# Optimization experiments

Hardware: AMD Instinct MI355X
Metric: run time of the kernel (lower is better)

## Reference

```python
import jax, jax.numpy as jnp
import numpy as np

MARGIN = 0.2
NEG_INF = -1e9  # safe stand-in for -inf when masking the max


def setup_inputs() -> dict:
    key = jax.random.key(0)
    k1, k2, k3 = jax.random.split(key, 3)
    B, D = 8192, 256
    p = jax.random.normal(k1, (B, D), dtype=jnp.float32)
    # module docstring says projections are normalized
    projections = p / jnp.linalg.norm(p, axis=1, keepdims=True)
    affordance_ids = jax.random.randint(k2, (B,), 0, 36, dtype=jnp.int64)
    instance_ids = jax.random.randint(k3, (B,), 0, 2048, dtype=jnp.int64)
    return {
        "projections": projections,
        "affordance_ids": affordance_ids,
        "instance_ids": instance_ids,
    }


def reference(projections, affordance_ids, instance_ids):
    # (B, B) cosine similarities
    sim = jnp.matmul(projections, projections.T)

    aff_eq = affordance_ids[:, None] == affordance_ids[None, :]
    inst_eq = instance_ids[:, None] == instance_ids[None, :]
    pos_mask = aff_eq & ~inst_eq          # same affordance, different instance
    neg_mask = ~aff_eq                    # different affordance

    # per-row hard negative: max similarity over negatives
    hard_neg = jnp.max(jnp.where(neg_mask, sim, NEG_INF), axis=1)  # (B,)

    # rows contribute only if they have >=1 positive AND >=1 negative
    valid_row = pos_mask.any(axis=1) & neg_mask.any(axis=1)        # (B,)
    pair_mask = pos_mask & valid_row[:, None]                      # (B, B)

    # margin loss for every (anchor i, positive j) pair
    losses = jnp.maximum(hard_neg[:, None] - sim + MARGIN, 0.0)

    total = jnp.sum(jnp.where(pair_mask, losses, 0.0))
    num_pairs = jnp.sum(pair_mask)
    return jnp.where(num_pairs > 0, total / num_pairs, 0.0)
```

## Files before the change

kernel.cpp:

```cpp
#include <hip/hip_runtime.h>

#define NB 8192
#define ND 256
#define NCLS 64
#define LOSS_MARGIN 0.2f
#define NEG_INF_F (-1e9f)
#define LMAXT 3
#define NBLK_LOSS (NCLS * LMAXT * LMAXT)
#define NT 64
#define NTILE_T 2080

typedef __attribute__((ext_vector_type(8))) __bf16 bf16x8;
typedef __attribute__((ext_vector_type(4))) float f32x4;

__device__ __forceinline__ unsigned short f2bf(float f) {
  unsigned u = __float_as_uint(f);
  unsigned r = (u + 0x7fffu + ((u >> 16) & 1u)) >> 16;
  return (unsigned short)r;
}

__device__ __forceinline__ void gl_lds16(const void* gsrc, void* ldst) {
  __builtin_amdgcn_global_load_lds(
      (const __attribute__((address_space(1))) void*)gsrc,
      (__attribute__((address_space(3))) void*)ldst, 16, 0, 0);
}

__global__ __launch_bounds__(256) void build_idx(const int* __restrict__ aff,
                                                 int* __restrict__ class_start,
                                                 int* __restrict__ class_idx) {
  const int c = blockIdx.x;
  const int t = threadIdx.x;
  const int lane = t & 63, wave = t >> 6;
  __shared__ int wtotLT[4];
  __shared__ int wtotEQ[4];

  int a[32];
#pragma unroll
  for (int k = 0; k < 32; ++k) a[k] = aff[t * 32 + k];
  int ltc = 0, meq = 0;
#pragma unroll
  for (int k = 0; k < 32; ++k) {
    ltc += (a[k] < c) ? 1 : 0;
    meq += (a[k] == c) ? 1 : 0;
  }

  int sc = meq;
  for (int d = 1; d < 64; d <<= 1) {
    int n = __shfl_up(sc, d);
    if (lane >= d) sc += n;
  }
  int ltr = ltc;
  for (int off = 32; off; off >>= 1) ltr += __shfl_down(ltr, off);
  if (lane == 63) wtotEQ[wave] = sc;
  if (lane == 0) wtotLT[wave] = ltr;
  __syncthreads();

  int base = wtotLT[0] + wtotLT[1] + wtotLT[2] + wtotLT[3];
  int wpre = 0;
  for (int w = 0; w < wave; ++w) wpre += wtotEQ[w];
  int p = base + wpre + (sc - meq);

  if (t == 0) {
    class_start[c] = base;
    if (c == 0) class_start[NCLS] = NB;
  }
#pragma unroll
  for (int k = 0; k < 32; ++k)
    if (a[k] == c) class_idx[p++] = t * 32 + k;
}

__global__ __launch_bounds__(256) void gather_convert(const float* __restrict__ P,
                                                      const int* __restrict__ aff,
                                                      const int* __restrict__ inst,
                                                      const int* __restrict__ class_idx,
                                                      unsigned short* __restrict__ Psort,
                                                      int* __restrict__ affSort,
                                                      int* __restrict__ instSort) {
  const int t = threadIdx.x;
  const int sr = blockIdx.x * 8 + (t >> 5);
  const int c = t & 31;
  const int src = class_idx[sr];
  const float4* ps = (const float4*)(P + (size_t)src * ND);
  ushort4* pd = (ushort4*)(Psort + (size_t)sr * ND);
#pragma unroll
  for (int q = 0; q < 2; ++q) {
    float4 v = ps[c + q * 32];
    ushort4 h;
    h.x = f2bf(v.x); h.y = f2bf(v.y); h.z = f2bf(v.z); h.w = f2bf(v.w);
    pd[c + q * 32] = h;
  }
  if (c == 0) {
    affSort[sr] = aff[src];
    instSort[sr] = inst[src];
  }
}

__global__ __launch_bounds__(256, 4) void simmax_mfma(const unsigned short* __restrict__ Psort,
                                                      const int* __restrict__ affSort,
                                                      float* __restrict__ part) {
  int wg = blockIdx.x;
  wg = (wg & 7) * (NTILE_T / 8) + (wg >> 3);
  int bi = (int)((129.0f - sqrtf(129.0f * 129.0f - 8.0f * (float)wg)) * 0.5f);
  while (bi * 64 - bi * (bi - 1) / 2 > wg) --bi;
  while ((bi + 1) * 64 - (bi + 1) * bi / 2 <= wg) ++bi;
  const int bj = bi + (wg - (bi * 64 - bi * (bi - 1) / 2));

  __shared__ __align__(16) unsigned short smemu[16384];
  float* rowmax_s = (float*)&smemu[0];
  float* colmax_s = (float*)&smemu[512];

  const int t = threadIdx.x;
  const int lane = t & 63;
  const int wave = t >> 6;
  const int r0 = bi * 128, c0 = bj * 128;

  const bool needMask = (affSort[c0] <= affSort[r0 + 127]);

  const int wr = (wave >> 1) * 64;
  const int wc = (wave & 1) * 64;

  f32x4 acc[4][4];
#pragma unroll
  for (int m = 0; m < 4; ++m)
#pragma unroll
    for (int n = 0; n < 4; ++n) acc[m][n] = (f32x4){0.f, 0.f, 0.f, 0.f};

  const int ci0 = t, ci1 = 256 + t;
  const int kg0 = ci0 >> 7, rw0 = ci0 & 127;
  const int kg1 = ci1 >> 7, rw1 = ci1 & 127;

#define STAGE_SIM(B, KC)                                                      \
  do {                                                                        \
    gl_lds16(Psort + (size_t)(r0 + rw0) * ND + (KC) + kg0 * 8,                \
             &smemu[(B) * 4096 + ci0 * 8]);                                   \
    gl_lds16(Psort + (size_t)(c0 + rw0) * ND + (KC) + kg0 * 8,                \
             &smemu[8192 + (B) * 4096 + ci0 * 8]);                            \
    gl_lds16(Psort + (size_t)(r0 + rw1) * ND + (KC) + kg1 * 8,                \
             &smemu[(B) * 4096 + ci1 * 8]);                                   \
    gl_lds16(Psort + (size_t)(c0 + rw1) * ND + (KC) + kg1 * 8,                \
             &smemu[8192 + (B) * 4096 + ci1 * 8]);                            \
  } while (0)

  STAGE_SIM(0, 0);
  asm volatile("s_waitcnt vmcnt(0) lgkmcnt(0)" ::: "memory");
  __builtin_amdgcn_s_barrier();
  __builtin_amdgcn_sched_barrier(0);

  int cur = 0;
#pragma unroll 1
  for (int s = 0; s < 8; ++s) {
    if (s < 7) STAGE_SIM(cur ^ 1, (s + 1) * 32);
    const int kg = lane >> 4, lr = lane & 15;
    bf16x8 a[4], b[4];
#pragma unroll
    for (int m = 0; m < 4; ++m)
      a[m] = *(const bf16x8*)&smemu[cur * 4096 + (kg * 128 + wr + m * 16 + lr) * 8];
#pragma unroll
    for (int n = 0; n < 4; ++n)
      b[n] = *(const bf16x8*)&smemu[8192 + cur * 4096 + (kg * 128 + wc + n * 16 + lr) * 8];
#pragma unroll
    for (int m = 0; m < 4; ++m)
#pragma unroll
      for (int n = 0; n < 4; ++n)
        acc[m][n] = __builtin_amdgcn_mfma_f32_16x16x32_bf16(a[m], b[n], acc[m][n], 0, 0, 0);
    __builtin_amdgcn_sched_barrier(0);
    if (s < 7) {
      asm volatile("s_waitcnt vmcnt(0)" ::: "memory");
      __builtin_amdgcn_s_barrier();
      __builtin_amdgcn_sched_barrier(0);
    }
    cur ^= 1;
  }

  if (needMask) {
    int aj[4];
#pragma unroll
    for (int n = 0; n < 4; ++n) aj[n] = affSort[c0 + wc + n * 16 + (lane & 15)];
#pragma unroll
    for (int m = 0; m < 4; ++m) {
#pragma unroll
      for (int r = 0; r < 4; ++r) {
        const int lrow = wr + m * 16 + (lane >> 4) * 4 + r;
        const int ai = affSort[r0 + lrow];
        float rmax = NEG_INF_F;
#pragma unroll
        for (int n = 0; n < 4; ++n)
          if (aj[n] != ai) rmax = fmaxf(rmax, acc[m][n][r]);
        rmax = fmaxf(rmax, __shfl_xor(rmax, 1));
        rmax = fmaxf(rmax, __shfl_xor(rmax, 2));
        rmax = fmaxf(rmax, __shfl_xor(rmax, 4));
        rmax = fmaxf(rmax, __shfl_xor(rmax, 8));
        if ((lane & 15) == 0) rowmax_s[lrow * 2 + (wc >> 6)] = rmax;
      }
    }
    if (bi != bj) {
#pragma unroll
      for (int n = 0; n < 4; ++n) {
        const int lcol = wc + n * 16 + (lane & 15);
        float cmax = NEG_INF_F;
#pragma unroll
        for (int m = 0; m < 4; ++m) {
          const int lrb = wr + m * 16 + (lane >> 4) * 4;
#pragma unroll
          for (int r = 0; r < 4; ++r)
            if (affSort[r0 + lrb + r] != aj[n]) cmax = fmaxf(cmax, acc[m][n][r]);
        }
        cmax = fmaxf(cmax, __shfl_xor(cmax, 16));
        cmax = fmaxf(cmax, __shfl_xor(cmax, 32));
        if (lane < 16) colmax_s[lcol * 2 + (wr >> 6)] = cmax;
      }
    }
  } else {
#pragma unroll
    for (int m = 0; m < 4; ++m) {
#pragma unroll
      for (int r = 0; r < 4; ++r) {
        float rmax = fmaxf(fmaxf(acc[m][0][r], acc[m][1][r]),
                           fmaxf(acc[m][2][r], acc[m][3][r]));
        rmax = fmaxf(rmax, __shfl_xor(rmax, 1));
        rmax = fmaxf(rmax, __shfl_xor(rmax, 2));
        rmax = fmaxf(rmax, __shfl_xor(rmax, 4));
        rmax = fmaxf(rmax, __shfl_xor(rmax, 8));
        if ((lane & 15) == 0)
          rowmax_s[(wr + m * 16 + (lane >> 4) * 4 + r) * 2 + (wc >> 6)] = rmax;
      }
    }
#pragma unroll
    for (int n = 0; n < 4; ++n) {
      float cmax = NEG_INF_F;
#pragma unroll
      for (int m = 0; m < 4; ++m)
#pragma unroll
        for (int r = 0; r < 4; ++r) cmax = fmaxf(cmax, acc[m][n][r]);
      cmax = fmaxf(cmax, __shfl_xor(cmax, 16));
      cmax = fmaxf(cmax, __shfl_xor(cmax, 32));
      if (lane < 16) colmax_s[(wc + n * 16 + (lane & 15)) * 2 + (wr >> 6)] = cmax;
    }
  }
  __syncthreads();
  if (t < 128) {
    part[(size_t)bj * NB + (r0 + t)] = fmaxf(rowmax_s[t * 2], rowmax_s[t * 2 + 1]);
  } else if (bi != bj) {
    const int cc = t - 128;
    part[(size_t)bi * NB + (c0 + cc)] = fmaxf(colmax_s[cc * 2], colmax_s[cc * 2 + 1]);
  }
#undef STAGE_SIM
}

__global__ __launch_bounds__(256) void hn_reduce(const float* __restrict__ part,
                                                 float* __restrict__ hn) {
  const int i = blockIdx.x * 256 + threadIdx.x;
  float m = NEG_INF_F;
#pragma unroll 16
  for (int q = 0; q < NT; ++q) m = fmaxf(m, part[(size_t)q * NB + i]);
  hn[i] = m;
}

__global__ __launch_bounds__(256, 4) void loss_mfma(const unsigned short* __restrict__ Psort,
                                                    const int* __restrict__ class_start,
                                                    const int* __restrict__ instSort,
                                                    const float* __restrict__ hn,
                                                    float* __restrict__ bsum,
                                                    int* __restrict__ bcnt) {
  const int c = blockIdx.z;
  const int ti = blockIdx.x, tj = blockIdx.y;
  const int bid = (c * LMAXT + ti) * LMAXT + tj;
  const int t = threadIdx.x;
  const int base = class_start[c];
  const int cnt = class_start[c + 1] - base;
  const int nt = (cnt + 127) >> 7;
  if (ti >= nt || tj >= nt || cnt >= NB) {
    if (t == 0) { bsum[bid] = 0.f; bcnt[bid] = 0; }
    return;
  }

  __shared__ __align__(16) unsigned short At[2][4096];
  __shared__ __align__(16) unsigned short Bt[2][4096];
  __shared__ int instI[128], instJ[128];
  __shared__ float hnI[128];

  const int lane = t & 63;
  const int wave = t >> 6;

  if (t < 128) {
    int ri = ti * 128 + t;
    int gi = base + (ri < cnt ? ri : 0);
    instI[t] = instSort[gi];
    hnI[t] = hn[gi];
  } else {
    int tt = t - 128;
    int rj = tj * 128 + tt;
    int gj = base + (rj < cnt ? rj : 0);
    instJ[tt] = instSort[gj];
  }

  const int wr = (wave >> 1) * 64;
  const int wc = (wave & 1) * 64;

  f32x4 acc[4][4];
#pragma unroll
  for (int m = 0; m < 4; ++m)
#pragma unroll
    for (int n = 0; n < 4; ++n) acc[m][n] = (f32x4){0.f, 0.f, 0.f, 0.f};

  const int ci0 = t, ci1 = 256 + t;
  const int kg0 = ci0 >> 7, rw0 = ci0 & 127;
  const int kg1 = ci1 >> 7, rw1 = ci1 & 127;
  const int ra0 = base + (ti * 128 + rw0 < cnt ? ti * 128 + rw0 : 0);
  const int ra1 = base + (ti * 128 + rw1 < cnt ? ti * 128 + rw1 : 0);
  const int rb0 = base + (tj * 128 + rw0 < cnt ? tj * 128 + rw0 : 0);
  const int rb1 = base + (tj * 128 + rw1 < cnt ? tj * 128 + rw1 : 0);

#define STAGE_LOSS(B, KC)                                               \
  do {                                                                  \
    gl_lds16(Psort + (size_t)ra0 * ND + (KC) + kg0 * 8, &At[B][ci0 * 8]); \
    gl_lds16(Psort + (size_t)rb0 * ND + (KC) + kg0 * 8, &Bt[B][ci0 * 8]); \
    gl_lds16(Psort + (size_t)ra1 * ND + (KC) + kg1 * 8, &At[B][ci1 * 8]); \
    gl_lds16(Psort + (size_t)rb1 * ND + (KC) + kg1 * 8, &Bt[B][ci1 * 8]); \
  } while (0)

  STAGE_LOSS(0, 0);
  asm volatile("s_waitcnt vmcnt(0) lgkmcnt(0)" ::: "memory");
  __builtin_amdgcn_s_barrier();
  __builtin_amdgcn_sched_barrier(0);

  int cur = 0;
#pragma unroll 1
  for (int s = 0; s < 8; ++s) {
    if (s < 7) STAGE_LOSS(cur ^ 1, (s + 1) * 32);
    const int kg = lane >> 4, lr = lane & 15;
    bf16x8 a[4], b[4];
#pragma unroll
    for (int m = 0; m < 4; ++m)
      a[m] = *(const bf16x8*)&At[cur][(kg * 128 + wr + m * 16 + lr) * 8];
#pragma unroll
    for (int n = 0; n < 4; ++n)
      b[n] = *(const bf16x8*)&Bt[cur][(kg * 128 + wc + n * 16 + lr) * 8];
#pragma unroll
    for (int m = 0; m < 4; ++m)
#pragma unroll
      for (int n = 0; n < 4; ++n)
        acc[m][n] = __builtin_amdgcn_mfma_f32_16x16x32_bf16(a[m], b[n], acc[m][n], 0, 0, 0);
    __builtin_amdgcn_sched_barrier(0);
    if (s < 7) {
      asm volatile("s_waitcnt vmcnt(0)" ::: "memory");
      __builtin_amdgcn_s_barrier();
      __builtin_amdgcn_sched_barrier(0);
    }
    cur ^= 1;
  }

  float lsum = 0.f;
  int lcnt = 0;
#pragma unroll
  for (int m = 0; m < 4; ++m) {
#pragma unroll
    for (int r = 0; r < 4; ++r) {
      const int lrow = wr + m * 16 + (lane >> 4) * 4 + r;
      const int ri = ti * 128 + lrow;
      if (ri >= cnt) continue;
      const float hnv = hnI[lrow];
      const int ii = instI[lrow];
#pragma unroll
      for (int n = 0; n < 4; ++n) {
        const int lcol = wc + n * 16 + (lane & 15);
        const int rj = tj * 128 + lcol;
        if (rj < cnt && instJ[lcol] != ii) {
          lsum += fmaxf(hnv - acc[m][n][r] + LOSS_MARGIN, 0.f);
          lcnt += 1;
        }
      }
    }
  }

  for (int off = 32; off; off >>= 1) {
    lsum += __shfl_down(lsum, off);
    lcnt += __shfl_down(lcnt, off);
  }
  __shared__ float wsum[4];
  __shared__ int wcnt[4];
  if (lane == 0) { wsum[wave] = lsum; wcnt[wave] = lcnt; }
  __syncthreads();
  if (t == 0) {
    bsum[bid] = wsum[0] + wsum[1] + wsum[2] + wsum[3];
    bcnt[bid] = wcnt[0] + wcnt[1] + wcnt[2] + wcnt[3];
  }
#undef STAGE_LOSS
}

__global__ __launch_bounds__(256) void finalize_kernel(const float* __restrict__ bsum,
                                                       const int* __restrict__ bcnt,
                                                       float* __restrict__ out) {
  const int t = threadIdx.x;
  float s = 0.f;
  int n = 0;
  for (int i = t; i < NBLK_LOSS; i += 256) { s += bsum[i]; n += bcnt[i]; }
  for (int off = 32; off; off >>= 1) {
    s += __shfl_down(s, off);
    n += __shfl_down(n, off);
  }
  __shared__ float wsum[4];
  __shared__ int wcnt[4];
  if ((t & 63) == 0) { wsum[t >> 6] = s; wcnt[t >> 6] = n; }
  __syncthreads();
  if (t == 0) {
    const float S = wsum[0] + wsum[1] + wsum[2] + wsum[3];
    const int N = wcnt[0] + wcnt[1] + wcnt[2] + wcnt[3];
    out[0] = (N > 0) ? (S / (float)N) : 0.0f;
  }
}

extern "C" void kernel_launch(void* const* d_in, const int* in_sizes, int n_in,
                              void* d_out, int out_size, void* d_ws, size_t ws_size,
                              hipStream_t stream) {
  const float* P = (const float*)d_in[0];
  const int* aff = (const int*)d_in[1];
  const int* inst = (const int*)d_in[2];
  float* out = (float*)d_out;

  unsigned short* Psort = (unsigned short*)d_ws;
  float* part = (float*)((char*)d_ws + (size_t)NB * ND * 2);
  int* ibase = (int*)((char*)part + (size_t)NT * NB * 4);
  float* hn        = (float*)ibase;
  int* class_start = ibase + NB;
  int* class_idx   = ibase + NB + NCLS + 1;
  int* affSort     = ibase + 2 * NB + NCLS + 1;
  int* instSort    = ibase + 3 * NB + NCLS + 1;
  float* bsum = (float*)(ibase + 4 * NB + NCLS + 1);
  int* bcnt   = ibase + 4 * NB + NCLS + 1 + NBLK_LOSS;

  build_idx<<<NCLS, 256, 0, stream>>>(aff, class_start, class_idx);
  gather_convert<<<NB / 8, 256, 0, stream>>>(P, aff, inst, class_idx, Psort,
                                             affSort, instSort);
  simmax_mfma<<<NTILE_T, 256, 0, stream>>>(Psort, affSort, part);
  hn_reduce<<<NB / 256, 256, 0, stream>>>(part, hn);
  loss_mfma<<<dim3(LMAXT, LMAXT, NCLS), 256, 0, stream>>>(Psort, class_start, instSort,
                                                          hn, bsum, bcnt);
  finalize_kernel<<<1, 256, 0, stream>>>(bsum, bcnt, out);
}
```

Measured before the change: 89.48 us.

## Process two triangular sim tiles per workgroup, prefetching second tile during first

The similarity-max kernel now handles two consecutive upper-triangle tiles per workgroup, launching half as many blocks. During the last k-step of tile A it issues the first k-slice load of tile B, so B's first global fetch overlaps A's final MFMAs and epilogue. Row and column max scratch moves to dedicated shared arrays so the epilogue does not clobber the staging buffers holding B's prefetched data. This trades grid parallelism (1040 blocks across 256 CUs) for amortised launch and prologue latency, and could leave load imbalance in the final wave.

Result: slower. 100.8 us (+12.6%).

```diff
diff --git a/kernel.cpp b/kernel.cpp
--- a/kernel.cpp
+++ b/kernel.cpp
@@ -9,6 +9,7 @@
 #define NBLK_LOSS (NCLS * LMAXT * LMAXT)
 #define NT 64
 #define NTILE_T 2080
+#define NPAIR 1040
 
 typedef __attribute__((ext_vector_type(8))) __bf16 bf16x8;
 typedef __attribute__((ext_vector_type(4))) float f32x4;
@@ -23,6 +24,14 @@
   __builtin_amdgcn_global_load_lds(
       (const __attribute__((address_space(1))) void*)gsrc,
       (__attribute__((address_space(3))) void*)ldst, 16, 0, 0);
+}
+
+__device__ __forceinline__ void tri_decode(int wg, int& bi, int& bj) {
+  int b = (int)((129.0f - sqrtf(129.0f * 129.0f - 8.0f * (float)wg)) * 0.5f);
+  while (b * 64 - b * (b - 1) / 2 > wg) --b;
+  while ((b + 1) * 64 - (b + 1) * b / 2 <= wg) ++b;
+  bi = b;
+  bj = b + (wg - (b * 64 - b * (b - 1) / 2));
 }
 
 __global__ __launch_bounds__(256) void build_idx(const int* __restrict__ aff,
@@ -98,50 +107,153 @@
 __global__ __launch_bounds__(256, 4) void simmax_mfma(const unsigned short* __restrict__ Psort,
                                                       const int* __restrict__ affSort,
                                                       float* __restrict__ part) {
-  int wg = blockIdx.x;
-  wg = (wg & 7) * (NTILE_T / 8) + (wg >> 3);
-  int bi = (int)((129.0f - sqrtf(129.0f * 129.0f - 8.0f * (float)wg)) * 0.5f);
-  while (bi * 64 - bi * (bi - 1) / 2 > wg) --bi;
-  while ((bi + 1) * 64 - (bi + 1) * bi / 2 <= wg) ++bi;
-  const int bj = bi + (wg - (bi * 64 - bi * (bi - 1) / 2));
+  int b = blockIdx.x;
+  b = (b & 7) * (NPAIR / 8) + (b >> 3);
+  int biA, bjA, biB, bjB;
+  tri_decode(2 * b, biA, bjA);
+  tri_decode(2 * b + 1, biB, bjB);
 
   __shared__ __align__(16) unsigned short smemu[16384];
-  float* rowmax_s = (float*)&smemu[0];
-  float* colmax_s = (float*)&smemu[512];
+  __shared__ float rowmax_s[128][2];
+  __shared__ float colmax_s[128][2];
 
   const int t = threadIdx.x;
   const int lane = t & 63;
   const int wave = t >> 6;
-  const int r0 = bi * 128, c0 = bj * 128;
-
-  const bool needMask = (affSort[c0] <= affSort[r0 + 127]);
+
+  const int r0a = biA * 128, c0a = bjA * 128;
+  const int r0b = biB * 128, c0b = bjB * 128;
+
+  const bool needMaskA = (affSort[c0a] <= affSort[r0a + 127]);
+  const bool needMaskB = (affSort[c0b] <= affSort[r0b + 127]);
 
   const int wr = (wave >> 1) * 64;
   const int wc = (wave & 1) * 64;
 
   f32x4 acc[4][4];
-#pragma unroll
-  for (int m = 0; m < 4; ++m)
-#pragma unroll
-    for (int n = 0; n < 4; ++n) acc[m][n] = (f32x4){0.f, 0.f, 0.f, 0.f};
 
   const int ci0 = t, ci1 = 256 + t;
   const int kg0 = ci0 >> 7, rw0 = ci0 & 127;
   const int kg1 = ci1 >> 7, rw1 = ci1 & 127;
 
-#define STAGE_SIM(B, KC)                                                      \
+#define STAGE_SIM(B, R0, C0, KC)                                              \
   do {                                                                        \
-    gl_lds16(Psort + (size_t)(r0 + rw0) * ND + (KC) + kg0 * 8,                \
+    gl_lds16(Psort + (size_t)((R0) + rw0) * ND + (KC) + kg0 * 8,              \
              &smemu[(B) * 4096 + ci0 * 8]);                                   \
-    gl_lds16(Psort + (size_t)(c0 + rw0) * ND + (KC) + kg0 * 8,                \
+    gl_lds16(Psort + (size_t)((C0) + rw0) * ND + (KC) + kg0 * 8,              \
              &smemu[8192 + (B) * 4096 + ci0 * 8]);                            \
-    gl_lds16(Psort + (size_t)(r0 + rw1) * ND + (KC) + kg1 * 8,                \
+    gl_lds16(Psort + (size_t)((R0) + rw1) * ND + (KC) + kg1 * 8,              \
              &smemu[(B) * 4096 + ci1 * 8]);                                   \
-    gl_lds16(Psort + (size_t)(c0 + rw1) * ND + (KC) + kg1 * 8,                \
+    gl_lds16(Psort + (size_t)((C0) + rw1) * ND + (KC) + kg1 * 8,              \
              &smemu[8192 + (B) * 4096 + ci1 * 8]);                            \
   } while (0)
 
-  STAGE_SIM(0, 0);
+#define KBODY(CUR)                                                            \
+  do {                                                                        \
+    const int kg = lane >> 4, lr = lane & 15;                                 \
+    bf16x8 a[4], bfr[4];                                                      \
+    _Pragma("unroll")                                                         \
+    for (int m = 0; m < 4; ++m)                                               \
+      a[m] = *(const bf16x8*)&smemu[(CUR) * 4096 +                            \
+                                    (kg * 128 + wr + m * 16 + lr) * 8];       \
+    _Pragma("unroll")                                                         \
+    for (int n = 0; n < 4; ++n)                                               \
+      bfr[n] = *(const bf16x8*)&smemu[8192 + (CUR) * 4096 +                   \
+                                      (kg * 128 + wc + n * 16 + lr) * 8];     \
+    _Pragma("unroll")                                                         \
+    for (int m = 0; m < 4; ++m)                                               \
+      _Pragma("unroll")                                                       \
+      for (int n = 0; n < 4; ++n)                                             \
+        acc[m][n] = __builtin_amdgcn_mfma_f32_16x16x32_bf16(a[m], bfr[n],     \
+                                                            acc[m][n], 0, 0, 0); \
+  } while (0)
+
+#define EPILOG(R0, C0, BI, BJ, NEEDMASK)                                      \
+  do {                                                                        \
+    if (NEEDMASK) {                                                           \
+      int aj[4];                                                              \
+      _Pragma("unroll")                                                       \
+      for (int n = 0; n < 4; ++n)                                             \
+        aj[n] = affSort[(C0) + wc + n * 16 + (lane & 15)];                    \
+      _Pragma("unroll")                                                       \
+      for (int m = 0; m < 4; ++m) {                                           \
+        _Pragma("unroll")                                                     \
+        for (int r = 0; r < 4; ++r) {                                         \
+          const int lrow = wr + m * 16 + (lane >> 4) * 4 + r;                 \
+          const int ai = affSort[(R0) + lrow];                                \
+          float rmax = NEG_INF_F;                                             \
+          _Pragma("unroll")                                                   \
+          for (int n = 0; n < 4; ++n)                                         \
+            if (aj[n] != ai) rmax = fmaxf(rmax, acc[m][n][r]);                \
+          rmax = fmaxf(rmax, __shfl_xor(rmax, 1));                            \
+          rmax = fmaxf(rmax, __shfl_xor(rmax, 2));                            \
+          rmax = fmaxf(rmax, __shfl_xor(rmax, 4));                            \
+          rmax = fmaxf(rmax, __shfl_xor(rmax, 8));                            \
+          if ((lane & 15) == 0) rowmax_s[lrow][wc >> 6] = rmax;               \
+        }                                                                     \
+      }                                                                       \
+      if ((BI) != (BJ)) {                                                     \
+        _Pragma("unroll")                                                     \
+        for (int n = 0; n < 4; ++n) {                                         \
+          const int lcol = wc + n * 16 + (lane & 15);                         \
+          float cmax = NEG_INF_F;                                             \
+          _Pragma("unroll")                                                   \
+          for (int m = 0; m < 4; ++m) {                                       \
+            const int lrb = wr + m * 16 + (lane >> 4) * 4;                    \
+            _Pragma("unroll")                                                 \
+            for (int r = 0; r < 4; ++r)                                       \
+              if (affSort[(R0) + lrb + r] != aj[n])                           \
+                cmax = fmaxf(cmax, acc[m][n][r]);                             \
+          }                                                                   \
+          cmax = fmaxf(cmax, __shfl_xor(cmax, 16));                           \
+          cmax = fmaxf(cmax, __shfl_xor(cmax, 32));                           \
+          if (lane < 16) colmax_s[lcol][wr >> 6] = cmax;                      \
+        }                                                                     \
+      }                                                                       \
+    } else {                                                                  \
+      _Pragma("unroll")                                                       \
+      for (int m = 0; m < 4; ++m) {                                           \
+        _Pragma("unroll")                                                     \
+        for (int r = 0; r < 4; ++r) {                                         \
+          float rmax = fmaxf(fmaxf(acc[m][0][r], acc[m][1][r]),               \
+                             fmaxf(acc[m][2][r], acc[m][3][r]));              \
+          rmax = fmaxf(rmax, __shfl_xor(rmax, 1));                            \
+          rmax = fmaxf(rmax, __shfl_xor(rmax, 2));                            \
+          rmax = fmaxf(rmax, __shfl_xor(rmax, 4));                            \
+          rmax = fmaxf(rmax, __shfl_xor(rmax, 8));                            \
+          if ((lane & 15) == 0)                                               \
+            rowmax_s[wr + m * 16 + (lane >> 4) * 4 + r][wc >> 6] = rmax;      \
+        }                                                                     \
+      }                                                                       \
+      _Pragma("unroll")                                                       \
+      for (int n = 0; n < 4; ++n) {                                           \
+        float cmax = NEG_INF_F;                                               \
+        _Pragma("unroll")                                                     \
+        for (int m = 0; m < 4; ++m)                                           \
+          _Pragma("unroll")                                                   \
+          for (int r = 0; r < 4; ++r) cmax = fmaxf(cmax, acc[m][n][r]);       \
+        cmax = fmaxf(cmax, __shfl_xor(cmax, 16));                             \
+        cmax = fmaxf(cmax, __shfl_xor(cmax, 32));                             \
+        if (lane < 16) colmax_s[wc + n * 16 + (lane & 15)][wr >> 6] = cmax;   \
+      }                                                                       \
+    }                                                                         \
+    __syncthreads();                                                          \
+    if (t < 128) {                                                            \
+      part[(size_t)(BJ) * NB + ((R0) + t)] =                                  \
+          fmaxf(rowmax_s[t][0], rowmax_s[t][1]);                              \
+    } else if ((BI) != (BJ)) {                                                \
+      const int cc = t - 128;                                                 \
+      part[(size_t)(BI) * NB + ((C0) + cc)] =                                 \
+          fmaxf(colmax_s[cc][0], colmax_s[cc][1]);                            \
+    }                                                                         \
+  } while (0)
+
+#pragma unroll
+  for (int m = 0; m < 4; ++m)
+#pragma unroll
+    for (int n = 0; n < 4; ++n) acc[m][n] = (f32x4){0.f, 0.f, 0.f, 0.f};
+
+  STAGE_SIM(0, r0a, c0a, 0);
   asm volatile("s_waitcnt vmcnt(0) lgkmcnt(0)" ::: "memory");
   __builtin_amdgcn_s_barrier();
   __builtin_amdgcn_sched_barrier(0);
@@ -149,20 +261,9 @@
   int cur = 0;
 #pragma unroll 1
   for (int s = 0; s < 8; ++s) {
-    if (s < 7) STAGE_SIM(cur ^ 1, (s + 1) * 32);
-    const int kg = lane >> 4, lr = lane & 15;
-    bf16x8 a[4], b[4];
-#pragma unroll
-    for (int m = 0; m < 4; ++m)
-      a[m] = *(const bf16x8*)&smemu[cur * 4096 + (kg * 128 + wr + m * 16 + lr) * 8];
-#pragma unroll
-    for (int n = 0; n < 4; ++n)
-      b[n] = *(const bf16x8*)&smemu[8192 + cur * 4096 + (kg * 128 + wc + n * 16 + lr) * 8];
-#pragma unroll
-    for (int m = 0; m < 4; ++m)
-#pragma unroll
-      for (int n = 0; n < 4; ++n)
-        acc[m][n] = __builtin_amdgcn_mfma_f32_16x16x32_bf16(a[m], b[n], acc[m][n], 0, 0, 0);
+    if (s < 7) STAGE_SIM(cur ^ 1, r0a, c0a, (s + 1) * 32);
+    else       STAGE_SIM(cur ^ 1, r0b, c0b, 0);
+    KBODY(cur);
     __builtin_amdgcn_sched_barrier(0);
     if (s < 7) {
       asm volatile("s_waitcnt vmcnt(0)" ::: "memory");
@@ -172,78 +273,33 @@
     cur ^= 1;
   }
 
-  if (needMask) {
-    int aj[4];
-#pragma unroll
-    for (int n = 0; n < 4; ++n) aj[n] = affSort[c0 + wc + n * 16 + (lane & 15)];
-#pragma unroll
-    for (int m = 0; m < 4; ++m) {
-#pragma unroll
-      for (int r = 0; r < 4; ++r) {
-        const int lrow = wr + m * 16 + (lane >> 4) * 4 + r;
-        const int ai = affSort[r0 + lrow];
-        float rmax = NEG_INF_F;
-#pragma unroll
-        for (int n = 0; n < 4; ++n)
-          if (aj[n] != ai) rmax = fmaxf(rmax, acc[m][n][r]);
-        rmax = fmaxf(rmax, __shfl_xor(rmax, 1));
-        rmax = fmaxf(rmax, __shfl_xor(rmax, 2));
-        rmax = fmaxf(rmax, __shfl_xor(rmax, 4));
-        rmax = fmaxf(rmax, __shfl_xor(rmax, 8));
-        if ((lane & 15) == 0) rowmax_s[lrow * 2 + (wc >> 6)] = rmax;
-      }
+  EPILOG(r0a, c0a, biA, bjA, needMaskA);
+
+#pragma unroll
+  for (int m = 0; m < 4; ++m)
+#pragma unroll
+    for (int n = 0; n < 4; ++n) acc[m][n] = (f32x4){0.f, 0.f, 0.f, 0.f};
+
+  asm volatile("s_waitcnt vmcnt(0)" ::: "memory");
+  __builtin_amdgcn_s_barrier();
+  __builtin_amdgcn_sched_barrier(0);
+
+#pragma unroll 1
+  for (int s = 0; s < 8; ++s) {
+    if (s < 7) STAGE_SIM(cur ^ 1, r0b, c0b, (s + 1) * 32);
+    KBODY(cur);
+    __builtin_amdgcn_sched_barrier(0);
+    if (s < 7) {
+      asm volatile("s_waitcnt vmcnt(0)" ::: "memory");
+      __builtin_amdgcn_s_barrier();
+      __builtin_amdgcn_sched_barrier(0);
     }
-    if (bi != bj) {
-#pragma unroll
-      for (int n = 0; n < 4; ++n) {
-        const int lcol = wc + n * 16 + (lane & 15);
-        float cmax = NEG_INF_F;
-#pragma unroll
-        for (int m = 0; m < 4; ++m) {
-          const int lrb = wr + m * 16 + (lane >> 4) * 4;
-#pragma unroll
-          for (int r = 0; r < 4; ++r)
-            if (affSort[r0 + lrb + r] != aj[n]) cmax = fmaxf(cmax, acc[m][n][r]);
-        }
-        cmax = fmaxf(cmax, __shfl_xor(cmax, 16));
-        cmax = fmaxf(cmax, __shfl_xor(cmax, 32));
-        if (lane < 16) colmax_s[lcol * 2 + (wr >> 6)] = cmax;
-      }
-    }
-  } else {
-#pragma unroll
-    for (int m = 0; m < 4; ++m) {
-#pragma unroll
-      for (int r = 0; r < 4; ++r) {
-        float rmax = fmaxf(fmaxf(acc[m][0][r], acc[m][1][r]),
-                           fmaxf(acc[m][2][r], acc[m][3][r]));
-        rmax = fmaxf(rmax, __shfl_xor(rmax, 1));
-        rmax = fmaxf(rmax, __shfl_xor(rmax, 2));
-        rmax = fmaxf(rmax, __shfl_xor(rmax, 4));
-        rmax = fmaxf(rmax, __shfl_xor(rmax, 8));
-        if ((lane & 15) == 0)
-          rowmax_s[(wr + m * 16 + (lane >> 4) * 4 + r) * 2 + (wc >> 6)] = rmax;
-      }
-    }
-#pragma unroll
-    for (int n = 0; n < 4; ++n) {
-      float cmax = NEG_INF_F;
-#pragma unroll
-      for (int m = 0; m < 4; ++m)
-#pragma unroll
-        for (int r = 0; r < 4; ++r) cmax = fmaxf(cmax, acc[m][n][r]);
-      cmax = fmaxf(cmax, __shfl_xor(cmax, 16));
-      cmax = fmaxf(cmax, __shfl_xor(cmax, 32));
-      if (lane < 16) colmax_s[(wc + n * 16 + (lane & 15)) * 2 + (wr >> 6)] = cmax;
-    }
-  }
-  __syncthreads();
-  if (t < 128) {
-    part[(size_t)bj * NB + (r0 + t)] = fmaxf(rowmax_s[t * 2], rowmax_s[t * 2 + 1]);
-  } else if (bi != bj) {
-    const int cc = t - 128;
-    part[(size_t)bi * NB + (c0 + cc)] = fmaxf(colmax_s[cc * 2], colmax_s[cc * 2 + 1]);
-  }
+    cur ^= 1;
+  }
+
+  EPILOG(r0b, c0b, biB, bjB, needMaskB);
+#undef EPILOG
+#undef KBODY
 #undef STAGE_SIM
 }
 
@@ -432,7 +488,7 @@
   build_idx<<<NCLS, 256, 0, stream>>>(aff, class_start, class_idx);
   gather_convert<<<NB / 8, 256, 0, stream>>>(P, aff, inst, class_idx, Psort,
                                              affSort, instSort);
-  simmax_mfma<<<NTILE_T, 256, 0, stream>>>(Psort, affSort, part);
+  simmax_mfma<<<NPAIR, 256, 0, stream>>>(Psort, affSort, part);
   hn_reduce<<<NB / 256, 256, 0, stream>>>(part, hn);
   loss_mfma<<<dim3(LMAXT, LMAXT, NCLS), 256, 0, stream>>>(Psort, class_start, instSort,
                                                           hn, bsum, bcnt);
```

## Cache near-diagonal similarity tiles in bf16 and reuse them for the loss

Applied to the files above, without the earlier changes.

The similarity kernel now writes bf16 copies of the masked tiles within four tile-diagonals of the main diagonal into a workspace buffer. The loss stage no longer runs a second MFMA pass. It becomes a scalar pair loop that gathers cached similarities for same-class, different-instance pairs. This removes the recomputed matmul, but adds 2-byte scattered stores in the similarity kernel and a latency-bound serial loop over rows. It also rounds the similarity to bf16 before computing the margin loss.

Result: slower. 129.1 us (+44.3%).

```diff
diff --git a/kernel.cpp b/kernel.cpp
--- a/kernel.cpp
+++ b/kernel.cpp
@@ -5,8 +5,7 @@
 #define NCLS 64
 #define LOSS_MARGIN 0.2f
 #define NEG_INF_F (-1e9f)
-#define LMAXT 3
-#define NBLK_LOSS (NCLS * LMAXT * LMAXT)
+#define NBLK_LOSS 256
 #define NT 64
 #define NTILE_T 2080
 
@@ -97,7 +96,8 @@
 
 __global__ __launch_bounds__(256, 4) void simmax_mfma(const unsigned short* __restrict__ Psort,
                                                       const int* __restrict__ affSort,
-                                                      float* __restrict__ part) {
+                                                      float* __restrict__ part,
+                                                      unsigned short* __restrict__ simbuf) {
   int wg = blockIdx.x;
   wg = (wg & 7) * (NTILE_T / 8) + (wg >> 3);
   int bi = (int)((129.0f - sqrtf(129.0f * 129.0f - 8.0f * (float)wg)) * 0.5f);
@@ -210,6 +210,22 @@
         if (lane < 16) colmax_s[lcol * 2 + (wr >> 6)] = cmax;
       }
     }
+    const int d = bj - bi;
+    if (d < 4) {
+      unsigned short* dst = simbuf + ((size_t)((bi << 2) + d) << 14);
+#pragma unroll
+      for (int m = 0; m < 4; ++m) {
+#pragma unroll
+        for (int r = 0; r < 4; ++r) {
+          const int lrow = wr + m * 16 + (lane >> 4) * 4 + r;
+#pragma unroll
+          for (int n = 0; n < 4; ++n) {
+            const int lcol = wc + n * 16 + (lane & 15);
+            dst[lrow * 128 + lcol] = f2bf(acc[m][n][r]);
+          }
+        }
+      }
+    }
   } else {
 #pragma unroll
     for (int m = 0; m < 4; ++m) {
@@ -256,117 +272,40 @@
   hn[i] = m;
 }
 
-__global__ __launch_bounds__(256, 4) void loss_mfma(const unsigned short* __restrict__ Psort,
-                                                    const int* __restrict__ class_start,
-                                                    const int* __restrict__ instSort,
-                                                    const float* __restrict__ hn,
-                                                    float* __restrict__ bsum,
-                                                    int* __restrict__ bcnt) {
-  const int c = blockIdx.z;
-  const int ti = blockIdx.x, tj = blockIdx.y;
-  const int bid = (c * LMAXT + ti) * LMAXT + tj;
-  const int t = threadIdx.x;
+__global__ __launch_bounds__(256) void loss_pairs(const int* __restrict__ class_start,
+                                                  const int* __restrict__ instSort,
+                                                  const float* __restrict__ hn,
+                                                  const unsigned short* __restrict__ simbuf,
+                                                  float* __restrict__ bsum,
+                                                  int* __restrict__ bcnt) {
+  const int c = blockIdx.y;
+  const int chunk = blockIdx.x;
+  const int bid = c * 4 + chunk;
+  const int t = threadIdx.x;
+  const int lane = t & 63, wave = t >> 6;
   const int base = class_start[c];
   const int cnt = class_start[c + 1] - base;
-  const int nt = (cnt + 127) >> 7;
-  if (ti >= nt || tj >= nt || cnt >= NB) {
-    if (t == 0) { bsum[bid] = 0.f; bcnt[bid] = 0; }
-    return;
-  }
-
-  __shared__ __align__(16) unsigned short At[2][4096];
-  __shared__ __align__(16) unsigned short Bt[2][4096];
-  __shared__ int instI[128], instJ[128];
-  __shared__ float hnI[128];
-
-  const int lane = t & 63;
-  const int wave = t >> 6;
-
-  if (t < 128) {
-    int ri = ti * 128 + t;
-    int gi = base + (ri < cnt ? ri : 0);
-    instI[t] = instSort[gi];
-    hnI[t] = hn[gi];
-  } else {
-    int tt = t - 128;
-    int rj = tj * 128 + tt;
-    int gj = base + (rj < cnt ? rj : 0);
-    instJ[tt] = instSort[gj];
-  }
-
-  const int wr = (wave >> 1) * 64;
-  const int wc = (wave & 1) * 64;
-
-  f32x4 acc[4][4];
-#pragma unroll
-  for (int m = 0; m < 4; ++m)
-#pragma unroll
-    for (int n = 0; n < 4; ++n) acc[m][n] = (f32x4){0.f, 0.f, 0.f, 0.f};
-
-  const int ci0 = t, ci1 = 256 + t;
-  const int kg0 = ci0 >> 7, rw0 = ci0 & 127;
-  const int kg1 = ci1 >> 7, rw1 = ci1 & 127;
-  const int ra0 = base + (ti * 128 + rw0 < cnt ? ti * 128 + rw0 : 0);
-  const int ra1 = base + (ti * 128 + rw1 < cnt ? ti * 128 + rw1 : 0);
-  const int rb0 = base + (tj * 128 + rw0 < cnt ? tj * 128 + rw0 : 0);
-  const int rb1 = base + (tj * 128 + rw1 < cnt ? tj * 128 + rw1 : 0);
-
-#define STAGE_LOSS(B, KC)                                               \
-  do {                                                                  \
-    gl_lds16(Psort + (size_t)ra0 * ND + (KC) + kg0 * 8, &At[B][ci0 * 8]); \
-    gl_lds16(Psort + (size_t)rb0 * ND + (KC) + kg0 * 8, &Bt[B][ci0 * 8]); \
-    gl_lds16(Psort + (size_t)ra1 * ND + (KC) + kg1 * 8, &At[B][ci1 * 8]); \
-    gl_lds16(Psort + (size_t)rb1 * ND + (KC) + kg1 * 8, &Bt[B][ci1 * 8]); \
-  } while (0)
-
-  STAGE_LOSS(0, 0);
-  asm volatile("s_waitcnt vmcnt(0) lgkmcnt(0)" ::: "memory");
-  __builtin_amdgcn_s_barrier();
-  __builtin_amdgcn_sched_barrier(0);
-
-  int cur = 0;
-#pragma unroll 1
-  for (int s = 0; s < 8; ++s) {
-    if (s < 7) STAGE_LOSS(cur ^ 1, (s + 1) * 32);
-    const int kg = lane >> 4, lr = lane & 15;
-    bf16x8 a[4], b[4];
-#pragma unroll
-    for (int m = 0; m < 4; ++m)
-      a[m] = *(const bf16x8*)&At[cur][(kg * 128 + wr + m * 16 + lr) * 8];
-#pragma unroll
-    for (int n = 0; n < 4; ++n)
-      b[n] = *(const bf16x8*)&Bt[cur][(kg * 128 + wc + n * 16 + lr) * 8];
-#pragma unroll
-    for (int m = 0; m < 4; ++m)
-#pragma unroll
-      for (int n = 0; n < 4; ++n)
-        acc[m][n] = __builtin_amdgcn_mfma_f32_16x16x32_bf16(a[m], b[n], acc[m][n], 0, 0, 0);
-    __builtin_amdgcn_sched_barrier(0);
-    if (s < 7) {
-      asm volatile("s_waitcnt vmcnt(0)" ::: "memory");
-      __builtin_amdgcn_s_barrier();
-      __builtin_amdgcn_sched_barrier(0);
-    }
-    cur ^= 1;
-  }
 
   float lsum = 0.f;
   int lcnt = 0;
-#pragma unroll
-  for (int m = 0; m < 4; ++m) {
-#pragma unroll
-    for (int r = 0; r < 4; ++r) {
-      const int lrow = wr + m * 16 + (lane >> 4) * 4 + r;
-      const int ri = ti * 128 + lrow;
-      if (ri >= cnt) continue;
-      const float hnv = hnI[lrow];
-      const int ii = instI[lrow];
-#pragma unroll
-      for (int n = 0; n < 4; ++n) {
-        const int lcol = wc + n * 16 + (lane & 15);
-        const int rj = tj * 128 + lcol;
-        if (rj < cnt && instJ[lcol] != ii) {
-          lsum += fmaxf(hnv - acc[m][n][r] + LOSS_MARGIN, 0.f);
+
+  if (cnt < NB) {
+#pragma unroll 1
+    for (int ri = chunk; ri < cnt; ri += 4) {
+      const int gi = base + ri;
+      const float hnv = hn[gi];
+      const int ii = instSort[gi];
+#pragma unroll 1
+      for (int rj = t; rj < cnt; rj += 256) {
+        if (rj == ri) continue;
+        const int gj = base + rj;
+        if (instSort[gj] != ii) {
+          const int lo = min(gi, gj), hi = max(gi, gj);
+          const int b0 = lo >> 7, d = (hi >> 7) - b0;
+          const unsigned short sb =
+              simbuf[((size_t)((b0 << 2) + d) << 14) + ((lo & 127) << 7) + (hi & 127)];
+          const float s = __uint_as_float((unsigned)sb << 16);
+          lsum += fmaxf(hnv - s + LOSS_MARGIN, 0.f);
           lcnt += 1;
         }
       }
@@ -385,16 +324,14 @@
     bsum[bid] = wsum[0] + wsum[1] + wsum[2] + wsum[3];
     bcnt[bid] = wcnt[0] + wcnt[1] + wcnt[2] + wcnt[3];
   }
-#undef STAGE_LOSS
 }
 
 __global__ __launch_bounds__(256) void finalize_kernel(const float* __restrict__ bsum,
                                                        const int* __restrict__ bcnt,
                                                        float* __restrict__ out) {
   const int t = threadIdx.x;
-  float s = 0.f;
-  int n = 0;
-  for (int i = t; i < NBLK_LOSS; i += 256) { s += bsum[i]; n += bcnt[i]; }
+  float s = bsum[t];
+  int n = bcnt[t];
   for (int off = 32; off; off >>= 1) {
     s += __shfl_down(s, off);
     n += __shfl_down(n, off);
@@ -420,7 +357,9 @@
 
   unsigned short* Psort = (unsigned short*)d_ws;
   float* part = (float*)((char*)d_ws + (size_t)NB * ND * 2);
-  int* ibase = (int*)((char*)part + (size_t)NT * NB * 4);
+  unsigned short* simbuf =
+      (unsigned short*)((char*)part + (size_t)NT * NB * 4);
+  int* ibase = (int*)((char*)simbuf + (size_t)256 * 16384 * 2);
   float* hn        = (float*)ibase;
   int* class_start = ibase + NB;
   int* class_idx   = ibase + NB + NCLS + 1;
@@ -432,9 +371,9 @@
   build_idx<<<NCLS, 256, 0, stream>>>(aff, class_start, class_idx);
   gather_convert<<<NB / 8, 256, 0, stream>>>(P, aff, inst, class_idx, Psort,
                                              affSort, instSort);
-  simmax_mfma<<<NTILE_T, 256, 0, stream>>>(Psort, affSort, part);
+  simmax_mfma<<<NTILE_T, 256, 0, stream>>>(Psort, affSort, part, simbuf);
   hn_reduce<<<NB / 256, 256, 0, stream>>>(part, hn);
-  loss_mfma<<<dim3(LMAXT, LMAXT, NCLS), 256, 0, stream>>>(Psort, class_start, instSort,
-                                                          hn, bsum, bcnt);
+  loss_pairs<<<dim3(4, NCLS), 256, 0, stream>>>(class_start, instSort, hn,
+                                                simbuf, bsum, bcnt);
   finalize_kernel<<<1, 256, 0, stream>>>(bsum, bcnt, out);
 }
```

## Fuse hard-negative reduce and finalize into loss kernel via atomics

Applied to the files above, without the earlier changes.

Removes the separate hn_reduce and finalize kernels. The loss kernel now reduces the per-row partial maxima for its own rows, and the last block to finish, counted with an atomic, writes the final mean. Each block adds its partial sum to a fixed-point 64-bit atomic accumulator. This cuts two kernel launches and a global round trip, but the same 64-way partial reduction is now repeated in each tile that shares a row, and the fixed-point scaling can lose precision.

Measured after the change: 95.28 us. 1.06x slower.

```diff
diff --git a/kernel.cpp b/kernel.cpp
--- a/kernel.cpp
+++ b/kernel.cpp
@@ -6,7 +6,7 @@
 #define LOSS_MARGIN 0.2f
 #define NEG_INF_F (-1e9f)
 #define LMAXT 3
-#define NBLK_LOSS (NCLS * LMAXT * LMAXT)
+#define NBLK_LOSS (LMAXT * LMAXT * NCLS)
 #define NT 64
 #define NTILE_T 2080
 
@@ -27,12 +27,21 @@
 
 __global__ __launch_bounds__(256) void build_idx(const int* __restrict__ aff,
                                                  int* __restrict__ class_start,
-                                                 int* __restrict__ class_idx) {
+                                                 int* __restrict__ class_idx,
+                                                 unsigned long long* __restrict__ acc_sum,
+                                                 int* __restrict__ acc_cnt,
+                                                 int* __restrict__ acc_done) {
   const int c = blockIdx.x;
   const int t = threadIdx.x;
   const int lane = t & 63, wave = t >> 6;
   __shared__ int wtotLT[4];
   __shared__ int wtotEQ[4];
+
+  if (c == 0 && t == 0) {
+    *acc_sum = 0ull;
+    *acc_cnt = 0;
+    *acc_done = 0;
+  }
 
   int a[32];
 #pragma unroll
@@ -247,69 +256,64 @@
 #undef STAGE_SIM
 }
 
-__global__ __launch_bounds__(256) void hn_reduce(const float* __restrict__ part,
-                                                 float* __restrict__ hn) {
-  const int i = blockIdx.x * 256 + threadIdx.x;
-  float m = NEG_INF_F;
-#pragma unroll 16
-  for (int q = 0; q < NT; ++q) m = fmaxf(m, part[(size_t)q * NB + i]);
-  hn[i] = m;
-}
-
 __global__ __launch_bounds__(256, 4) void loss_mfma(const unsigned short* __restrict__ Psort,
                                                     const int* __restrict__ class_start,
                                                     const int* __restrict__ instSort,
-                                                    const float* __restrict__ hn,
-                                                    float* __restrict__ bsum,
-                                                    int* __restrict__ bcnt) {
+                                                    const float* __restrict__ part,
+                                                    unsigned long long* __restrict__ acc_sum,
+                                                    int* __restrict__ acc_cnt,
+                                                    int* __restrict__ acc_done,
+                                                    float* __restrict__ out) {
   const int c = blockIdx.z;
   const int ti = blockIdx.x, tj = blockIdx.y;
-  const int bid = (c * LMAXT + ti) * LMAXT + tj;
   const int t = threadIdx.x;
   const int base = class_start[c];
   const int cnt = class_start[c + 1] - base;
   const int nt = (cnt + 127) >> 7;
-  if (ti >= nt || tj >= nt || cnt >= NB) {
-    if (t == 0) { bsum[bid] = 0.f; bcnt[bid] = 0; }
-    return;
-  }
+  const bool active = (ti < nt) && (tj < nt) && (cnt < NB);
 
   __shared__ __align__(16) unsigned short At[2][4096];
   __shared__ __align__(16) unsigned short Bt[2][4096];
   __shared__ int instI[128], instJ[128];
   __shared__ float hnI[128];
+  __shared__ float wsum[4];
+  __shared__ int wcnt[4];
 
   const int lane = t & 63;
   const int wave = t >> 6;
 
-  if (t < 128) {
-    int ri = ti * 128 + t;
-    int gi = base + (ri < cnt ? ri : 0);
-    instI[t] = instSort[gi];
-    hnI[t] = hn[gi];
-  } else {
-    int tt = t - 128;
-    int rj = tj * 128 + tt;
-    int gj = base + (rj < cnt ? rj : 0);
-    instJ[tt] = instSort[gj];
-  }
-
-  const int wr = (wave >> 1) * 64;
-  const int wc = (wave & 1) * 64;
-
-  f32x4 acc[4][4];
-#pragma unroll
-  for (int m = 0; m < 4; ++m)
-#pragma unroll
-    for (int n = 0; n < 4; ++n) acc[m][n] = (f32x4){0.f, 0.f, 0.f, 0.f};
-
-  const int ci0 = t, ci1 = 256 + t;
-  const int kg0 = ci0 >> 7, rw0 = ci0 & 127;
-  const int kg1 = ci1 >> 7, rw1 = ci1 & 127;
-  const int ra0 = base + (ti * 128 + rw0 < cnt ? ti * 128 + rw0 : 0);
-  const int ra1 = base + (ti * 128 + rw1 < cnt ? ti * 128 + rw1 : 0);
-  const int rb0 = base + (tj * 128 + rw0 < cnt ? tj * 128 + rw0 : 0);
-  const int rb1 = base + (tj * 128 + rw1 < cnt ? tj * 128 + rw1 : 0);
+  if (active) {
+    if (t < 128) {
+      int ri = ti * 128 + t;
+      int gi = base + (ri < cnt ? ri : 0);
+      instI[t] = instSort[gi];
+      float m = NEG_INF_F;
+#pragma unroll 16
+      for (int q = 0; q < NT; ++q) m = fmaxf(m, part[(size_t)q * NB + gi]);
+      hnI[t] = m;
+    } else {
+      int tt = t - 128;
+      int rj = tj * 128 + tt;
+      int gj = base + (rj < cnt ? rj : 0);
+      instJ[tt] = instSort[gj];
+    }
+
+    const int wr = (wave >> 1) * 64;
+    const int wc = (wave & 1) * 64;
+
+    f32x4 acc[4][4];
+#pragma unroll
+    for (int m = 0; m < 4; ++m)
+#pragma unroll
+      for (int n = 0; n < 4; ++n) acc[m][n] = (f32x4){0.f, 0.f, 0.f, 0.f};
+
+    const int ci0 = t, ci1 = 256 + t;
+    const int kg0 = ci0 >> 7, rw0 = ci0 & 127;
+    const int kg1 = ci1 >> 7, rw1 = ci1 & 127;
+    const int ra0 = base + (ti * 128 + rw0 < cnt ? ti * 128 + rw0 : 0);
+    const int ra1 = base + (ti * 128 + rw1 < cnt ? ti * 128 + rw1 : 0);
+    const int rb0 = base + (tj * 128 + rw0 < cnt ? tj * 128 + rw0 : 0);
+    const int rb1 = base + (tj * 128 + rw1 < cnt ? tj * 128 + rw1 : 0);
 
 #define STAGE_LOSS(B, KC)                                               \
   do {                                                                  \
@@ -319,94 +323,86 @@
     gl_lds16(Psort + (size_t)rb1 * ND + (KC) + kg1 * 8, &Bt[B][ci1 * 8]); \
   } while (0)
 
-  STAGE_LOSS(0, 0);
-  asm volatile("s_waitcnt vmcnt(0) lgkmcnt(0)" ::: "memory");
-  __builtin_amdgcn_s_barrier();
-  __builtin_amdgcn_sched_barrier(0);
-
-  int cur = 0;
+    STAGE_LOSS(0, 0);
+    asm volatile("s_waitcnt vmcnt(0) lgkmcnt(0)" ::: "memory");
+    __builtin_amdgcn_s_barrier();
+    __builtin_amdgcn_sched_barrier(0);
+
+    int cur = 0;
 #pragma unroll 1
-  for (int s = 0; s < 8; ++s) {
-    if (s < 7) STAGE_LOSS(cur ^ 1, (s + 1) * 32);
-    const int kg = lane >> 4, lr = lane & 15;
-    bf16x8 a[4], b[4];
-#pragma unroll
-    for (int m = 0; m < 4; ++m)
-      a[m] = *(const bf16x8*)&At[cur][(kg * 128 + wr + m * 16 + lr) * 8];
-#pragma unroll
-    for (int n = 0; n < 4; ++n)
-      b[n] = *(const bf16x8*)&Bt[cur][(kg * 128 + wc + n * 16 + lr) * 8];
-#pragma unroll
-    for (int m = 0; m < 4; ++m)
+    for (int s = 0; s < 8; ++s) {
+      if (s < 7) STAGE_LOSS(cur ^ 1, (s + 1) * 32);
+      const int kg = lane >> 4, lr = lane & 15;
+      bf16x8 a[4], b[4];
+#pragma unroll
+      for (int m = 0; m < 4; ++m)
+        a[m] = *(const bf16x8*)&At[cur][(kg * 128 + wr + m * 16 + lr) * 8];
 #pragma unroll
       for (int n = 0; n < 4; ++n)
-        acc[m][n] = __builtin_amdgcn_mfma_f32_16x16x32_bf16(a[m], b[n], acc[m][n], 0, 0, 0);
-    __builtin_amdgcn_sched_barrier(0);
-    if (s < 7) {
-      asm volatile("s_waitcnt vmcnt(0)" ::: "memory");
-      __builtin_amdgcn_s_barrier();
+        b[n] = *(const bf16x8*)&Bt[cur][(kg * 128 + wc + n * 16 + lr) * 8];
+#pragma unroll
+      for (int m = 0; m < 4; ++m)
+#pragma unroll
+        for (int n = 0; n < 4; ++n)
+          acc[m][n] = __builtin_amdgcn_mfma_f32_16x16x32_bf16(a[m], b[n], acc[m][n], 0, 0, 0);
       __builtin_amdgcn_sched_barrier(0);
-    }
-    cur ^= 1;
-  }
-
-  float lsum = 0.f;
-  int lcnt = 0;
-#pragma unroll
-  for (int m = 0; m < 4; ++m) {
-#pragma unroll
-    for (int r = 0; r < 4; ++r) {
-      const int lrow = wr + m * 16 + (lane >> 4) * 4 + r;
-      const int ri = ti * 128 + lrow;
-      if (ri >= cnt) continue;
-      const float hnv = hnI[lrow];
-      const int ii = instI[lrow];
-#pragma unroll
-      for (int n = 0; n < 4; ++n) {
-        const int lcol = wc + n * 16 + (lane & 15);
-        const int rj = tj * 128 + lcol;
-        if (rj < cnt && instJ[lcol] != ii) {
-          lsum += fmaxf(hnv - acc[m][n][r] + LOSS_MARGIN, 0.f);
-          lcnt += 1;
+      if (s < 7) {
+        asm volatile("s_waitcnt vmcnt(0)" ::: "memory");
+        __builtin_amdgcn_s_barrier();
+        __builtin_amdgcn_sched_barrier(0);
+      }
+      cur ^= 1;
+    }
+#undef STAGE_LOSS
+
+    float lsum = 0.f;
+    int lcnt = 0;
+#pragma unroll
+    for (int m = 0; m < 4; ++m) {
+#pragma unroll
+      for (int r = 0; r < 4; ++r) {
+        const int lrow = wr + m * 16 + (lane >> 4) * 4 + r;
+        const int ri = ti * 128 + lrow;
+        if (ri >= cnt) continue;
+        const float hnv = hnI[lrow];
+        const int ii = instI[lrow];
+#pragma unroll
+        for (int n = 0; n < 4; ++n) {
+          const int lcol = wc + n * 16 + (lane & 15);
+          const int rj = tj * 128 + lcol;
+          if (rj < cnt && instJ[lcol] != ii) {
+            lsum += fmaxf(hnv - acc[m][n][r] + LOSS_MARGIN, 0.f);
+            lcnt += 1;
+          }
         }
       }
     }
-  }
-
-  for (int off = 32; off; off >>= 1) {
-    lsum += __shfl_down(lsum, off);
-    lcnt += __shfl_down(lcnt, off);
-  }
-  __shared__ float wsum[4];
-  __shared__ int wcnt[4];
-  if (lane == 0) { wsum[wave] = lsum; wcnt[wave] = lcnt; }
-  __syncthreads();
+
+    for (int off = 32; off; off >>= 1) {
+      lsum += __shfl_down(lsum, off);
+      lcnt += __shfl_down(lcnt, off);
+    }
+    if (lane == 0) { wsum[wave] = lsum; wcnt[wave] = lcnt; }
+    __syncthreads();
+  }
+
   if (t == 0) {
-    bsum[bid] = wsum[0] + wsum[1] + wsum[2] + wsum[3];
-    bcnt[bid] = wcnt[0] + wcnt[1] + wcnt[2] + wcnt[3];
-  }
-#undef STAGE_LOSS
-}
-
-__global__ __launch_bounds__(256) void finalize_kernel(const float* __restrict__ bsum,
-                                                       const int* __restrict__ bcnt,
-                                                       float* __restrict__ out) {
-  const int t = threadIdx.x;
-  float s = 0.f;
-  int n = 0;
-  for (int i = t; i < NBLK_LOSS; i += 256) { s += bsum[i]; n += bcnt[i]; }
-  for (int off = 32; off; off >>= 1) {
-    s += __shfl_down(s, off);
-    n += __shfl_down(n, off);
-  }
-  __shared__ float wsum[4];
-  __shared__ int wcnt[4];
-  if ((t & 63) == 0) { wsum[t >> 6] = s; wcnt[t >> 6] = n; }
-  __syncthreads();
-  if (t == 0) {
-    const float S = wsum[0] + wsum[1] + wsum[2] + wsum[3];
-    const int N = wcnt[0] + wcnt[1] + wcnt[2] + wcnt[3];
-    out[0] = (N > 0) ? (S / (float)N) : 0.0f;
+    if (active) {
+      const float bs = wsum[0] + wsum[1] + wsum[2] + wsum[3];
+      const int bc = wcnt[0] + wcnt[1] + wcnt[2] + wcnt[3];
+      if (bc > 0) {
+        atomicAdd(acc_sum, (unsigned long long)llrintf(bs * 1048576.0f));
+        atomicAdd(acc_cnt, bc);
+      }
+    }
+    __threadfence();
+    const int old = atomicAdd(acc_done, 1);
+    if (old == NBLK_LOSS - 1) {
+      __threadfence();
+      const unsigned long long S = atomicAdd(acc_sum, 0ull);
+      const int N = atomicAdd(acc_cnt, 0);
+      out[0] = (N > 0) ? (float)((double)S / 1048576.0 / (double)N) : 0.0f;
+    }
   }
 }
 
@@ -421,20 +417,21 @@
   unsigned short* Psort = (unsigned short*)d_ws;
   float* part = (float*)((char*)d_ws + (size_t)NB * ND * 2);
   int* ibase = (int*)((char*)part + (size_t)NT * NB * 4);
-  float* hn        = (float*)ibase;
-  int* class_start = ibase + NB;
-  int* class_idx   = ibase + NB + NCLS + 1;
-  int* affSort     = ibase + 2 * NB + NCLS + 1;
-  int* instSort    = ibase + 3 * NB + NCLS + 1;
-  float* bsum = (float*)(ibase + 4 * NB + NCLS + 1);
-  int* bcnt   = ibase + 4 * NB + NCLS + 1 + NBLK_LOSS;
-
-  build_idx<<<NCLS, 256, 0, stream>>>(aff, class_start, class_idx);
+  int* class_start = ibase;
+  int* class_idx   = ibase + NCLS + 1;
+  int* affSort     = ibase + NCLS + 1 + NB;
+  int* instSort    = ibase + NCLS + 1 + 2 * NB;
+  unsigned long long* acc_sum =
+      (unsigned long long*)(((uintptr_t)(ibase + NCLS + 1 + 3 * NB) + 7) & ~(uintptr_t)7);
+  int* acc_cnt  = (int*)(acc_sum + 1);
+  int* acc_done = acc_cnt + 1;
+
+  build_idx<<<NCLS, 256, 0, stream>>>(aff, class_start, class_idx,
+                                      acc_sum, acc_cnt, acc_done);
   gather_convert<<<NB / 8, 256, 0, stream>>>(P, aff, inst, class_idx, Psort,
                                              affSort, instSort);
   simmax_mfma<<<NTILE_T, 256, 0, stream>>>(Psort, affSort, part);
-  hn_reduce<<<NB / 256, 256, 0, stream>>>(part, hn);
   loss_mfma<<<dim3(LMAXT, LMAXT, NCLS), 256, 0, stream>>>(Psort, class_start, instSort,
-                                                          hn, bsum, bcnt);
-  finalize_kernel<<<1, 256, 0, stream>>>(bsum, bcnt, out);
-}
+                                                          part, acc_sum, acc_cnt,
+                                                          acc_done, out);
+}
```
